# Performance work log

Measured on AMD Instinct MI355X. Metric: run time of the kernel, lower is better.

The kernel has to match this reference:

```python
import jax, jax.numpy as jnp
import numpy as np

B, T_IN, H, V, MAXLEN = 128, 256, 512, 32, 128


def gru_cell(x, h, Wih, Whh, bih, bhh):
    # torch GRU cell: gates ordered (r, z, n)
    gi = x @ Wih.T + bih            # [B, 3H]
    gh = h @ Whh.T + bhh            # [B, 3H]
    ir, iz, inn = jnp.split(gi, 3, axis=-1)
    hr, hz, hn = jnp.split(gh, 3, axis=-1)
    r = jax.nn.sigmoid(ir + hr)
    z = jax.nn.sigmoid(iz + hz)
    n = jnp.tanh(inn + r * hn)
    return (1.0 - z) * n + z * h


def run_gru_layer(xs, Wih, Whh, bih, bhh):
    # xs: [B, T, D] -> outputs [B, T, H], final hidden [B, H]
    h0 = jnp.zeros((xs.shape[0], Whh.shape[1]), xs.dtype)

    def step(h, x):
        hn = gru_cell(x, h, Wih, Whh, bih, bhh)
        return hn, hn

    hT, ys = jax.lax.scan(step, h0, jnp.swapaxes(xs, 0, 1))
    return jnp.swapaxes(ys, 0, 1), hT


def setup_inputs() -> dict:
    key = jax.random.key(0)
    ks = jax.random.split(key, 24)
    s = 1.0 / np.sqrt(H)

    def p(k, shape):
        return (jax.random.normal(k, shape, jnp.float32) * s).astype(jnp.float32)

    return {
        "x": jax.random.normal(ks[0], (B, T_IN, 2), jnp.float32),
        "emb": p(ks[1], (V, H)),
        # encoder GRU: layer0 input dim 2, layer1 input dim H
        "enc_Wih0": p(ks[2], (3 * H, 2)), "enc_Whh0": p(ks[3], (3 * H, H)),
        "enc_bih0": p(ks[4], (3 * H,)), "enc_bhh0": p(ks[5], (3 * H,)),
        "enc_Wih1": p(ks[6], (3 * H, H)), "enc_Whh1": p(ks[7], (3 * H, H)),
        "enc_bih1": p(ks[8], (3 * H,)), "enc_bhh1": p(ks[9], (3 * H,)),
        # decoder GRU: layer0 input dim 2H (embedded+context), layer1 input dim H
        "dec_Wih0": p(ks[10], (3 * H, 2 * H)), "dec_Whh0": p(ks[11], (3 * H, H)),
        "dec_bih0": p(ks[12], (3 * H,)), "dec_bhh0": p(ks[13], (3 * H,)),
        "dec_Wih1": p(ks[14], (3 * H, H)), "dec_Whh1": p(ks[15], (3 * H, H)),
        "dec_bih1": p(ks[16], (3 * H,)), "dec_bhh1": p(ks[17], (3 * H,)),
        "q_W": p(ks[18], (H, H)), "q_b": p(ks[19], (H,)),
        "out_W": p(ks[20], (V, H)), "out_b": p(ks[21], (V,)),
    }


def reference(x, emb,
              enc_Wih0, enc_Whh0, enc_bih0, enc_bhh0,
              enc_Wih1, enc_Whh1, enc_bih1, enc_bhh1,
              dec_Wih0, dec_Whh0, dec_bih0, dec_bhh0,
              dec_Wih1, dec_Whh1, dec_bih1, dec_bhh1,
              q_W, q_b, out_W, out_b):
    # ----- encoder: 2-layer GRU over trajectory points -----
    y0, h0 = run_gru_layer(x, enc_Wih0, enc_Whh0, enc_bih0, enc_bhh0)
    enc_outs, h1 = run_gru_layer(y0, enc_Wih1, enc_Whh1, enc_bih1, enc_bhh1)
    hidden0 = jnp.stack([h0, h1])                      # [L, B, H]
    bsz = x.shape[0]

    def step(carry, _):
        hidden, tok = carry                            # [L,B,H], [B] int
        embedded = emb[tok]                            # [B, H]
        query = hidden[-1] @ q_W.T + q_b               # [B, H]
        scores = jnp.einsum('bh,bth->bt', query, enc_outs)
        attn_w = jax.nn.softmax(scores, axis=-1)       # [B, T_in]
        context = jnp.einsum('bt,bth->bh', attn_w, enc_outs)
        rnn_in = jnp.concatenate([embedded, context], axis=-1)  # [B, 2H]
        g0 = gru_cell(rnn_in, hidden[0], dec_Wih0, dec_Whh0, dec_bih0, dec_bhh0)
        g1 = gru_cell(g0, hidden[1], dec_Wih1, dec_Whh1, dec_bih1, dec_bhh1)
        logits = g1 @ out_W.T + out_b                  # [B, V]
        tok_next = jnp.argmax(logits, axis=-1)
        return (jnp.stack([g0, g1]), tok_next), (logits, attn_w)

    tok0 = jnp.zeros((bsz,), jnp.int32)
    (hidden_f, _), (logits_seq, attn_seq) = jax.lax.scan(
        step, (hidden0, tok0), None, length=MAXLEN)
    vec_out = jnp.swapaxes(logits_seq, 0, 1)           # [B, max_len, V]
    attn = jnp.swapaxes(attn_seq, 0, 1)                # [B, max_len, T_in]
    return vec_out, hidden_f, attn
```

## Files before the change

kernel.cpp:

```cpp
#include <hip/hip_runtime.h>
#include <math.h>

#define BB 128
#define TT 256
#define HH 512
#define VV 32
#define MLEN 128
#define SLOT 65536

#define WT_OFF 0
#define QT_OFF 24576
#define PR_OFF 26624
#define SC_OFF 28416
#define SM_FLOATS 32512

typedef long long ll;

struct P {
    const float *x, *emb;
    const float *eWih0, *eWhh0, *ebih0, *ebhh0;
    const float *eWih1, *eWhh1, *ebih1, *ebhh1;
    const float *dWih0, *dWhh0, *dbih0, *dbhh0;
    const float *dWih1, *dWhh1, *dbih1, *dbhh1;
    const float *qW, *qb, *outW, *outb;
    float *ws;
    float *vecO, *hidO, *attnO;
};

__device__ __forceinline__ float sigf(float v) { return 1.0f / (1.0f + __expf(-v)); }

__device__ __forceinline__ float ldA(const float* p) {
    return __hip_atomic_load(p, __ATOMIC_RELAXED, __HIP_MEMORY_SCOPE_AGENT);
}
__device__ __forceinline__ void stA(float* p, float v) {
    __hip_atomic_store(p, v, __ATOMIC_RELAXED, __HIP_MEMORY_SCOPE_AGENT);
}
__device__ __forceinline__ int ldAi(const int* p) {
    return __hip_atomic_load(p, __ATOMIC_RELAXED, __HIP_MEMORY_SCOPE_AGENT);
}
__device__ __forceinline__ void stAi(int* p, int v) {
    __hip_atomic_store(p, v, __ATOMIC_RELAXED, __HIP_MEMORY_SCOPE_AGENT);
}

__device__ __forceinline__ void gbar(int* W, int target) {
    __syncthreads();
    if (threadIdx.x == 0) {
        int par = target & 1;
        int g = blockIdx.x & 15;
        int* gc = W + 32 + (par * 16 + g) * 32;
        if (__hip_atomic_fetch_add(gc, 1, __ATOMIC_RELAXED, __HIP_MEMORY_SCOPE_AGENT) == 15) {
            __hip_atomic_store(gc, 0, __ATOMIC_RELAXED, __HIP_MEMORY_SCOPE_AGENT);
            int* rc = W + 1056 + par * 32;
            if (__hip_atomic_fetch_add(rc, 1, __ATOMIC_RELAXED, __HIP_MEMORY_SCOPE_AGENT) == 15) {
                __hip_atomic_store(rc, 0, __ATOMIC_RELAXED, __HIP_MEMORY_SCOPE_AGENT);
                __hip_atomic_store(W, target, __ATOMIC_RELAXED, __HIP_MEMORY_SCOPE_AGENT);
            }
        }
        while (__hip_atomic_load(W, __ATOMIC_RELAXED, __HIP_MEMORY_SCOPE_AGENT) < target)
            __builtin_amdgcn_s_sleep(2);
    }
    __syncthreads();
}

__global__ __launch_bounds__(512, 1) void kmain(P p) {
    __shared__ __align__(16) float smu[SM_FLOATS];
    const int tid = threadIdx.x;
    const int lane = tid & 63;
    const int wv = tid >> 6;
    const int blk = blockIdx.x;

    int* W = (int*)p.ws;
    int* tok = W + 4096;
    float* f = (float*)p.ws + 8192;
    float* eh0 = f;
    float* eh1 = f + 2 * SLOT;
    float* inp = f + 4 * SLOT;
    float* qbm = f + 5 * SLOT;
    float* scoresB = f + 6 * SLOT;
    float* T = f + 6 * SLOT + SLOT / 2;
    float* xT = T + 3 * HH * VV;
    float* encO = f + (SLOT / 4) * 33;

    const float4* t4 = (const float4*)smu;
    const float4* t4q = (const float4*)(smu + QT_OFF);

    const int jg = blk >> 1;
    const int bh = blk & 1;
    const int b2 = bh * 64 + lane;
    int bar = 0;

    {
        stA(eh0 + blk * 1024 + tid, 0.0f);
        stA(eh0 + blk * 1024 + 512 + tid, 0.0f);
        if (tid < 256) {
            int idx = blk * 256 + tid;
            int t = idx >> 8, c = (idx >> 7) & 1, b = idx & 127;
            stA(xT + idx, p.x[((ll)b * TT + t) * 2 + c]);
        }
        if (tid < 192) {
            int unit = blk * 192 + tid;
            int v = unit & 31, gj = unit >> 5;
            const float* wrow = p.dWih0 + (ll)gj * 1024;
            const float* erow = p.emb + (ll)v * HH;
            float acc = 0.0f;
#pragma unroll 8
            for (int d = 0; d < HH; ++d) acc = fmaf(wrow[d], erow[d], acc);
            stA(T + unit, acc);
        }
#pragma unroll
        for (int jl = 0; jl < 4; ++jl)
            smu[QT_OFF + jl * 512 + tid] = p.qW[((ll)(jg * 4 + jl)) * HH + tid];
#pragma unroll
        for (int r = 0; r < 24; ++r) {
            int g = r >> 2, jl = r & 3, j = jg * 4 + jl;
            const float* src = (g < 3) ? (p.eWhh0 + (ll)(g * HH + j) * HH)
                                       : (p.eWih1 + (ll)((g - 3) * HH + j) * HH);
            smu[WT_OFF + r * 512 + tid] = src[tid];
        }
#pragma unroll
        for (int r = 0; r < 12; ++r) {
            int g = r >> 2, jl = r & 3, j = jg * 4 + jl;
            smu[WT_OFF + (24 + r) * 512 + tid] = p.eWhh1[(ll)(g * HH + j) * HH + tid];
        }
        gbar(W, ++bar);
    }

    for (int t = 0; t <= TT; ++t) {
        const float* h0s = eh0 + (((t + 1) & 1) ? SLOT : 0);
        float*       h0d = eh0 + ((t & 1) ? SLOT : 0);
        const float* h1s = eh1 + (((t + 1) & 1) ? SLOT : 0);
        float*       h1d = eh1 + ((t & 1) ? SLOT : 0);

        smu[PR_OFF + tid] = 0.0f;
        smu[PR_OFF + 512 + tid] = 0.0f;
        smu[PR_OFF + 1024 + tid] = 0.0f;
        if (tid < 256) smu[PR_OFF + 1536 + tid] = 0.0f;
        __syncthreads();

        {
            const int rotE = jg & 7;
            const int ds0 = wv * 64;
            float acc[36];
#pragma unroll
            for (int r = 0; r < 36; ++r) acc[r] = 0.0f;
            float av[2][8], bv[2][8];
            {
                const int d0c = ds0 + rotE * 8;
#pragma unroll
                for (int u = 0; u < 8; ++u) av[0][u] = ldA(h0s + (ll)(d0c + u) * BB + b2);
#pragma unroll
                for (int u = 0; u < 8; ++u) bv[0][u] = ldA(h1s + (ll)(d0c + u) * BB + b2);
            }
#pragma unroll
            for (int c = 0; c < 8; ++c) {
                const int cb = c & 1, pb = cb ^ 1;
                if (c < 7) {
                    const int dn = ds0 + ((c + 1 + rotE) & 7) * 8;
#pragma unroll
                    for (int u = 0; u < 8; ++u) av[pb][u] = ldA(h0s + (ll)(dn + u) * BB + b2);
#pragma unroll
                    for (int u = 0; u < 8; ++u) bv[pb][u] = ldA(h1s + (ll)(dn + u) * BB + b2);
                }
                const int db = ds0 + ((c + rotE) & 7) * 8;
#pragma unroll
                for (int h2 = 0; h2 < 2; ++h2) {
                    const int q4 = (db + h2 * 4) >> 2;
#pragma unroll
                    for (int r = 0; r < 24; ++r) {
                        float4 w = t4[r * 128 + q4];
                        acc[r] = fmaf(w.x, av[cb][h2 * 4 + 0], acc[r]);
                        acc[r] = fmaf(w.y, av[cb][h2 * 4 + 1], acc[r]);
                        acc[r] = fmaf(w.z, av[cb][h2 * 4 + 2], acc[r]);
                        acc[r] = fmaf(w.w, av[cb][h2 * 4 + 3], acc[r]);
                    }
#pragma unroll
                    for (int r = 0; r < 12; ++r) {
                        float4 w = t4[(24 + r) * 128 + q4];
                        acc[24 + r] = fmaf(w.x, bv[cb][h2 * 4 + 0], acc[24 + r]);
                        acc[24 + r] = fmaf(w.y, bv[cb][h2 * 4 + 1], acc[24 + r]);
                        acc[24 + r] = fmaf(w.z, bv[cb][h2 * 4 + 2], acc[24 + r]);
                        acc[24 + r] = fmaf(w.w, bv[cb][h2 * 4 + 3], acc[24 + r]);
                    }
                }
            }
#pragma unroll
            for (int r = 0; r < 24; ++r)
                unsafeAtomicAdd(&smu[PR_OFF + r * 64 + lane], acc[r]);
#pragma unroll
            for (int r = 0; r < 12; ++r) {
                int g = r >> 2;
                int prow = (g < 2) ? (12 + g * 4) : 24;
                unsafeAtomicAdd(&smu[PR_OFF + (prow + (r & 3)) * 64 + lane], acc[24 + r]);
            }
        }
        __syncthreads();

        if (wv < 4) {
            if (t < TT) {
                int jl = wv, j = jg * 4 + jl;
                float* pr = smu + PR_OFF;
                float hr = pr[(0 + jl) * 64 + lane] + p.ebhh0[j];
                float hz = pr[(4 + jl) * 64 + lane] + p.ebhh0[HH + j];
                float hn = pr[(8 + jl) * 64 + lane] + p.ebhh0[2 * HH + j];
                float x0 = xT[t * 256 + b2], x1 = xT[t * 256 + 128 + b2];
                float ir = fmaf(p.eWih0[j * 2], x0, fmaf(p.eWih0[j * 2 + 1], x1, p.ebih0[j]));
                float iz = fmaf(p.eWih0[(HH + j) * 2], x0, fmaf(p.eWih0[(HH + j) * 2 + 1], x1, p.ebih0[HH + j]));
                float in_ = fmaf(p.eWih0[(2 * HH + j) * 2], x0, fmaf(p.eWih0[(2 * HH + j) * 2 + 1], x1, p.ebih0[2 * HH + j]));
                float r = sigf(ir + hr), z = sigf(iz + hz);
                float n = tanhf(in_ + r * hn);
                float hp = ldA(h0s + (ll)j * BB + b2);
                stA(h0d + (ll)j * BB + b2, (1.0f - z) * n + z * hp);
            }
        } else if (t >= 1) {
            int jl = wv - 4, j = jg * 4 + jl;
            float* pr = smu + PR_OFF;
            float rs = pr[(12 + jl) * 64 + lane] + p.ebih1[j] + p.ebhh1[j];
            float zs = pr[(16 + jl) * 64 + lane] + p.ebih1[HH + j] + p.ebhh1[HH + j];
            float in1 = pr[(20 + jl) * 64 + lane] + p.ebih1[2 * HH + j];
            float hn1 = pr[(24 + jl) * 64 + lane] + p.ebhh1[2 * HH + j];
            float r = sigf(rs), z = sigf(zs);
            float n = tanhf(in1 + r * hn1);
            float hp = ldA(h1s + (ll)j * BB + b2);
            float hv = (1.0f - z) * n + z * hp;
            stA(h1d + (ll)j * BB + b2, hv);
            stA(encO + ((ll)(t - 1) * HH + j) * BB + b2, hv);
        }
        gbar(W, ++bar);
    }

    {
        const float* h1c = eh1;
        if (tid < 256) smu[PR_OFF + tid] = 0.0f;
#pragma unroll
        for (int r = 0; r < 12; ++r) {
            int g = r >> 2, jl = r & 3, j = jg * 4 + jl;
            smu[WT_OFF + r * 1024 + tid]              = p.dWih0[(ll)(g * HH + j) * 1024 + 512 + tid];
            smu[WT_OFF + r * 1024 + 512 + tid]        = p.dWhh0[(ll)(g * HH + j) * HH + tid];
            smu[WT_OFF + (12 + r) * 1024 + tid]       = p.dWih1[(ll)(g * HH + j) * HH + tid];
            smu[WT_OFF + (12 + r) * 1024 + 512 + tid] = p.dWhh1[(ll)(g * HH + j) * HH + tid];
        }
        __syncthreads();
        {
            const int ds0 = wv * 64;
            float acc[4] = {0, 0, 0, 0};
            float av[8];
            for (int c = 0; c < 8; ++c) {
                int db = ds0 + c * 8;
#pragma unroll
                for (int u = 0; u < 8; ++u) av[u] = ldA(h1c + (ll)(db + u) * BB + b2);
#pragma unroll
                for (int h2 = 0; h2 < 2; ++h2) {
                    int q4 = (db + h2 * 4) >> 2;
#pragma unroll
                    for (int jl = 0; jl < 4; ++jl) {
                        float4 w = t4q[jl * 128 + q4];
                        acc[jl] = fmaf(w.x, av[h2 * 4 + 0], acc[jl]);
                        acc[jl] = fmaf(w.y, av[h2 * 4 + 1], acc[jl]);
                        acc[jl] = fmaf(w.z, av[h2 * 4 + 2], acc[jl]);
                        acc[jl] = fmaf(w.w, av[h2 * 4 + 3], acc[jl]);
                    }
                }
            }
#pragma unroll
            for (int jl = 0; jl < 4; ++jl)
                unsafeAtomicAdd(&smu[PR_OFF + jl * 64 + lane], acc[jl]);
        }
        __syncthreads();
        if (wv < 4) {
            int j = jg * 4 + wv;
            stA(qbm + (ll)j * BB + b2, smu[PR_OFF + wv * 64 + lane] + p.qb[j]);
        }
        if (blk == 128 && tid < BB) stAi(tok + tid, 0);
        gbar(W, ++bar);
    }

    for (int s = 0; s < MLEN; ++s) {
        const float* h0s = eh0 + (((s + 1) & 1) ? SLOT : 0);
        float*       g0d = eh0 + ((s & 1) ? SLOT : 0);
        const float* h1s = eh1 + ((s & 1) ? SLOT : 0);
        float*       h1d = eh1 + (((s + 1) & 1) ? SLOT : 0);

        {
            const int rotA = jg & 7;
            const int t0 = (blk >> 1) * 2;
            if (tid < 128) smu[PR_OFF + tid] = 0.0f;
            __syncthreads();
            const int js = wv * 64;
            float a0 = 0.0f, a1 = 0.0f;
            float qv[2][8], e0[2][8], e1[2][8];
            {
                const int j0 = js + rotA * 8;
#pragma unroll
                for (int u = 0; u < 8; ++u) {
                    qv[0][u] = ldA(qbm + (ll)(j0 + u) * BB + b2);
                    e0[0][u] = encO[((ll)t0 * HH + j0 + u) * BB + b2];
                    e1[0][u] = encO[((ll)(t0 + 1) * HH + j0 + u) * BB + b2];
                }
            }
#pragma unroll
            for (int c = 0; c < 8; ++c) {
                const int cb = c & 1, pb = cb ^ 1;
                if (c < 7) {
                    const int jn = js + ((c + 1 + rotA) & 7) * 8;
#pragma unroll
                    for (int u = 0; u < 8; ++u) {
                        qv[pb][u] = ldA(qbm + (ll)(jn + u) * BB + b2);
                        e0[pb][u] = encO[((ll)t0 * HH + jn + u) * BB + b2];
                        e1[pb][u] = encO[((ll)(t0 + 1) * HH + jn + u) * BB + b2];
                    }
                }
#pragma unroll
                for (int u = 0; u < 8; ++u) {
                    a0 = fmaf(qv[cb][u], e0[cb][u], a0);
                    a1 = fmaf(qv[cb][u], e1[cb][u], a1);
                }
            }
            unsafeAtomicAdd(&smu[PR_OFF + lane], a0);
            unsafeAtomicAdd(&smu[PR_OFF + 64 + lane], a1);
            __syncthreads();
            if (wv < 2)
                stA(scoresB + (ll)(t0 + wv) * BB + b2, smu[PR_OFF + wv * 64 + lane]);
        }
        gbar(W, ++bar);

        {
            const int d0 = jg * 4;
            float sv[32];
            for (int i = 0; i < 32; ++i) {
                int k = (i + (jg & 31)) & 31;
                sv[k] = ldA(scoresB + (ll)(wv * 32 + k) * BB + b2);
            }
            if (tid < 256) smu[PR_OFF + tid] = 0.0f;
            float mp = sv[0];
#pragma unroll
            for (int k = 1; k < 32; ++k) mp = fmaxf(mp, sv[k]);
            smu[SC_OFF + wv * 64 + lane] = mp;
            __syncthreads();
            float m = smu[SC_OFF + lane];
#pragma unroll
            for (int u = 1; u < 8; ++u) m = fmaxf(m, smu[SC_OFF + u * 64 + lane]);
            float e[32], lp = 0.0f;
#pragma unroll
            for (int k = 0; k < 32; ++k) { e[k] = __expf(sv[k] - m); lp += e[k]; }
            smu[SC_OFF + 512 + wv * 64 + lane] = lp;
            __syncthreads();
            float l = smu[SC_OFF + 512 + lane];
#pragma unroll
            for (int u = 1; u < 8; ++u) l += smu[SC_OFF + 512 + u * 64 + lane];
            float rl = 1.0f / l;
            if (blk < 16 && wv == jg) {
#pragma unroll
                for (int k = 0; k < 32; ++k) smu[SC_OFF + 1024 + k * 65 + lane] = e[k] * rl;
            }
            float c4[4] = {0, 0, 0, 0};
            float ev[2][32];
#pragma unroll
            for (int u = 0; u < 8; ++u) {
                const float* Ep = encO + ((ll)(wv * 32 + u) * HH + d0) * BB + b2;
#pragma unroll
                for (int q = 0; q < 4; ++q) ev[0][u * 4 + q] = Ep[q * BB];
            }
#pragma unroll
            for (int kb = 0; kb < 4; ++kb) {
                const int cb = kb & 1, pb = cb ^ 1;
                if (kb < 3) {
#pragma unroll
                    for (int u = 0; u < 8; ++u) {
                        const float* Ep = encO + ((ll)(wv * 32 + (kb + 1) * 8 + u) * HH + d0) * BB + b2;
#pragma unroll
                        for (int q = 0; q < 4; ++q) ev[pb][u * 4 + q] = Ep[q * BB];
                    }
                }
#pragma unroll
                for (int u = 0; u < 8; ++u) {
                    const int k = kb * 8 + u;
                    c4[0] = fmaf(e[k], ev[cb][u * 4 + 0], c4[0]);
                    c4[1] = fmaf(e[k], ev[cb][u * 4 + 1], c4[1]);
                    c4[2] = fmaf(e[k], ev[cb][u * 4 + 2], c4[2]);
                    c4[3] = fmaf(e[k], ev[cb][u * 4 + 3], c4[3]);
                }
            }
#pragma unroll
            for (int kk = 0; kk < 4; ++kk)
                unsafeAtomicAdd(&smu[PR_OFF + kk * 64 + lane], c4[kk]);
            __syncthreads();
            if (tid < 256) {
                int kk = tid >> 6, ln = tid & 63;
                float l2 = smu[SC_OFF + 512 + ln];
#pragma unroll
                for (int u = 1; u < 8; ++u) l2 += smu[SC_OFF + 512 + u * 64 + ln];
                float val = smu[PR_OFF + kk * 64 + ln] / l2;
                stA(inp + (ll)(d0 + kk) * BB + bh * 64 + ln, val);
            }
            if (blk < 16) {
                int bi = tid >> 3, tj = tid & 7;
#pragma unroll
                for (int u = 0; u < 4; ++u) {
                    int tl = tj * 4 + u;
                    p.attnO[((ll)(bh * 64 + bi) * MLEN + s) * TT + jg * 32 + tl] = smu[SC_OFF + 1024 + tl * 65 + bi];
                }
            }
        }
        gbar(W, ++bar);

        {
            const int rotG = jg & 15;
            smu[PR_OFF + tid] = 0.0f;
            smu[PR_OFF + 512 + tid] = 0.0f;
            __syncthreads();
            const int ctxw = (wv < 4);
            const float* stream = ctxw ? inp : h0s;
            const int ds0 = (wv & 3) * 128;
            const int tb = ctxw ? 0 : 512;
            float acc[12];
#pragma unroll
            for (int r = 0; r < 12; ++r) acc[r] = 0.0f;
            float av[2][8];
            {
                const int d0c = ds0 + rotG * 8;
#pragma unroll
                for (int u = 0; u < 8; ++u) av[0][u] = ldA(stream + (ll)(d0c + u) * BB + b2);
            }
#pragma unroll
            for (int c = 0; c < 16; ++c) {
                const int cb = c & 1, pb = cb ^ 1;
                if (c < 15) {
                    const int dn = ds0 + ((c + 1 + rotG) & 15) * 8;
#pragma unroll
                    for (int u = 0; u < 8; ++u) av[pb][u] = ldA(stream + (ll)(dn + u) * BB + b2);
                }
                const int db = ds0 + ((c + rotG) & 15) * 8;
#pragma unroll
                for (int h2 = 0; h2 < 2; ++h2) {
                    const int q4 = (tb + db + h2 * 4) >> 2;
#pragma unroll
                    for (int r = 0; r < 12; ++r) {
                        float4 w = t4[r * 256 + q4];
                        acc[r] = fmaf(w.x, av[cb][h2 * 4 + 0], acc[r]);
                        acc[r] = fmaf(w.y, av[cb][h2 * 4 + 1], acc[r]);
                        acc[r] = fmaf(w.z, av[cb][h2 * 4 + 2], acc[r]);
                        acc[r] = fmaf(w.w, av[cb][h2 * 4 + 3], acc[r]);
                    }
                }
            }
#pragma unroll
            for (int r = 0; r < 12; ++r) {
                int g = r >> 2;
                int prow = (g < 2) ? g * 4 : (ctxw ? 8 : 12);
                unsafeAtomicAdd(&smu[PR_OFF + (prow + (r & 3)) * 64 + lane], acc[r]);
            }
            __syncthreads();
            if (wv < 4) {
                int jl = wv, j = jg * 4 + jl;
                float* pr = smu + PR_OFF;
                int tokb = ldAi(tok + b2);
                float rs = T[(ll)j * 32 + tokb] + pr[(0 + jl) * 64 + lane] + p.dbih0[j] + p.dbhh0[j];
                float zs = T[(ll)(HH + j) * 32 + tokb] + pr[(4 + jl) * 64 + lane] + p.dbih0[HH + j] + p.dbhh0[HH + j];
                float ins = T[(ll)(2 * HH + j) * 32 + tokb] + pr[(8 + jl) * 64 + lane] + p.dbih0[2 * HH + j];
                float hns = pr[(12 + jl) * 64 + lane] + p.dbhh0[2 * HH + j];
                float r = sigf(rs), z = sigf(zs);
                float n = tanhf(ins + r * hns);
                float hp = ldA(h0s + (ll)j * BB + b2);
                stA(g0d + (ll)j * BB + b2, (1.0f - z) * n + z * hp);
            }
        }
        gbar(W, ++bar);

        {
            const int rotG = jg & 15;
            smu[PR_OFF + tid] = 0.0f;
            smu[PR_OFF + 512 + tid] = 0.0f;
            __syncthreads();
            const int iw = (wv < 4);
            const float* stream = iw ? g0d : h1s;
            const int ds0 = (wv & 3) * 128;
            const int tb = iw ? 0 : 512;
            float acc[12];
#pragma unroll
            for (int r = 0; r < 12; ++r) acc[r] = 0.0f;
            float av[2][8];
            {
                const int d0c = ds0 + rotG * 8;
#pragma unroll
                for (int u = 0; u < 8; ++u) av[0][u] = ldA(stream + (ll)(d0c + u) * BB + b2);
            }
#pragma unroll
            for (int c = 0; c < 16; ++c) {
                const int cb = c & 1, pb = cb ^ 1;
                if (c < 15) {
                    const int dn = ds0 + ((c + 1 + rotG) & 15) * 8;
#pragma unroll
                    for (int u = 0; u < 8; ++u) av[pb][u] = ldA(stream + (ll)(dn + u) * BB + b2);
                }
                const int db = ds0 + ((c + rotG) & 15) * 8;
#pragma unroll
                for (int h2 = 0; h2 < 2; ++h2) {
                    const int q4 = (tb + db + h2 * 4) >> 2;
#pragma unroll
                    for (int r = 0; r < 12; ++r) {
                        float4 w = t4[(12 + r) * 256 + q4];
                        acc[r] = fmaf(w.x, av[cb][h2 * 4 + 0], acc[r]);
                        acc[r] = fmaf(w.y, av[cb][h2 * 4 + 1], acc[r]);
                        acc[r] = fmaf(w.z, av[cb][h2 * 4 + 2], acc[r]);
                        acc[r] = fmaf(w.w, av[cb][h2 * 4 + 3], acc[r]);
                    }
                }
            }
#pragma unroll
            for (int r = 0; r < 12; ++r) {
                int g = r >> 2;
                int prow = (g < 2) ? g * 4 : (iw ? 8 : 12);
                unsafeAtomicAdd(&smu[PR_OFF + (prow + (r & 3)) * 64 + lane], acc[r]);
            }
            __syncthreads();
            if (wv < 4) {
                int jl = wv, j = jg * 4 + jl;
                float* pr = smu + PR_OFF;
                float rs = pr[(0 + jl) * 64 + lane] + p.dbih1[j] + p.dbhh1[j];
                float zs = pr[(4 + jl) * 64 + lane] + p.dbih1[HH + j] + p.dbhh1[HH + j];
                float ins = pr[(8 + jl) * 64 + lane] + p.dbih1[2 * HH + j];
                float hns = pr[(12 + jl) * 64 + lane] + p.dbhh1[2 * HH + j];
                float r = sigf(rs), z = sigf(zs);
                float n = tanhf(ins + r * hns);
                float hp = ldA(h1s + (ll)j * BB + b2);
                stA(h1d + (ll)j * BB + b2, (1.0f - z) * n + z * hp);
            }
        }
        gbar(W, ++bar);

        {
            const int rotD = jg & 7;
            const float* h1c = h1d;
            if (tid < 256) smu[PR_OFF + tid] = 0.0f;
            __syncthreads();
            {
                const int ds0 = wv * 64;
                float acc4[4] = {0, 0, 0, 0};
                float av[2][8];
                {
                    const int d0c = ds0 + rotD * 8;
#pragma unroll
                    for (int u = 0; u < 8; ++u) av[0][u] = ldA(h1c + (ll)(d0c + u) * BB + b2);
                }
#pragma unroll
                for (int c = 0; c < 8; ++c) {
                    const int cb = c & 1, pb = cb ^ 1;
                    if (c < 7) {
                        const int dn = ds0 + ((c + 1 + rotD) & 7) * 8;
#pragma unroll
                        for (int u = 0; u < 8; ++u) av[pb][u] = ldA(h1c + (ll)(dn + u) * BB + b2);
                    }
                    const int db = ds0 + ((c + rotD) & 7) * 8;
#pragma unroll
                    for (int h2 = 0; h2 < 2; ++h2) {
                        const int q4 = (db + h2 * 4) >> 2;
#pragma unroll
                        for (int jl = 0; jl < 4; ++jl) {
                            float4 w = t4q[jl * 128 + q4];
                            acc4[jl] = fmaf(w.x, av[cb][h2 * 4 + 0], acc4[jl]);
                            acc4[jl] = fmaf(w.y, av[cb][h2 * 4 + 1], acc4[jl]);
                            acc4[jl] = fmaf(w.z, av[cb][h2 * 4 + 2], acc4[jl]);
                            acc4[jl] = fmaf(w.w, av[cb][h2 * 4 + 3], acc4[jl]);
                        }
                    }
                }
#pragma unroll
                for (int jl = 0; jl < 4; ++jl)
                    unsafeAtomicAdd(&smu[PR_OFF + jl * 64 + lane], acc4[jl]);
            }
            __syncthreads();
            if (wv < 4) {
                int j = jg * 4 + wv;
                stA(qbm + (ll)j * BB + b2, smu[PR_OFF + wv * 64 + lane] + p.qb[j]);
            }
            if (blk >= 128 && blk < 160) {
                __syncthreads();
                const int bb = (blk - 128) * 4;
#pragma unroll
                for (int i = 0; i < 4; ++i) {
                    int f2 = i * 512 + tid;
                    int d = f2 >> 2, bi2 = f2 & 3;
                    smu[SC_OFF + f2] = ldA(h1c + (ll)d * BB + bb + bi2);
                }
                __syncthreads();
                if (tid < 128) {
                    const int bl = tid >> 5, v = tid & 31;
                    float acc = 0.0f;
                    for (int d4 = 0; d4 < 128; ++d4) {
                        float4 w4 = *(const float4*)(p.outW + (ll)v * HH + d4 * 4);
                        acc = fmaf(w4.x, smu[SC_OFF + (d4 * 4 + 0) * 4 + bl], acc);
                        acc = fmaf(w4.y, smu[SC_OFF + (d4 * 4 + 1) * 4 + bl], acc);
                        acc = fmaf(w4.z, smu[SC_OFF + (d4 * 4 + 2) * 4 + bl], acc);
                        acc = fmaf(w4.w, smu[SC_OFF + (d4 * 4 + 3) * 4 + bl], acc);
                    }
                    acc += p.outb[v];
                    p.vecO[((ll)(bb + bl) * MLEN + s) * VV + v] = acc;
                    smu[SC_OFF + 2048 + tid] = acc;
                }
                __syncthreads();
                if (tid < 4) {
                    int base = SC_OFF + 2048 + tid * 32;
                    float best = smu[base];
                    int bi2 = 0;
#pragma unroll
                    for (int u = 1; u < 32; ++u) {
                        float val = smu[base + u];
                        if (val > best) { best = val; bi2 = u; }
                    }
                    stAi(tok + bb + tid, bi2);
                }
            }
        }
        gbar(W, ++bar);
    }

    {
        int idx = blk * 512 + tid;
        int l = idx >> 16, rr = idx & 65535;
        int b = rr >> 9, h = rr & 511;
        const float* src = l ? eh1 : (eh0 + SLOT);
        p.hidO[idx] = ldA(src + (ll)h * BB + b);
    }
}

extern "C" void kernel_launch(void* const* d_in, const int* in_sizes, int n_in,
                              void* d_out, int out_size, void* d_ws, size_t ws_size,
                              hipStream_t stream) {
    (void)in_sizes; (void)n_in; (void)out_size; (void)ws_size;
    P prm;
    prm.x     = (const float*)d_in[0];
    prm.emb   = (const float*)d_in[1];
    prm.eWih0 = (const float*)d_in[2];
    prm.eWhh0 = (const float*)d_in[3];
    prm.ebih0 = (const float*)d_in[4];
    prm.ebhh0 = (const float*)d_in[5];
    prm.eWih1 = (const float*)d_in[6];
    prm.eWhh1 = (const float*)d_in[7];
    prm.ebih1 = (const float*)d_in[8];
    prm.ebhh1 = (const float*)d_in[9];
    prm.dWih0 = (const float*)d_in[10];
    prm.dWhh0 = (const float*)d_in[11];
    prm.dbih0 = (const float*)d_in[12];
    prm.dbhh0 = (const float*)d_in[13];
    prm.dWih1 = (const float*)d_in[14];
    prm.dWhh1 = (const float*)d_in[15];
    prm.dbih1 = (const float*)d_in[16];
    prm.dbhh1 = (const float*)d_in[17];
    prm.qW    = (const float*)d_in[18];
    prm.qb    = (const float*)d_in[19];
    prm.outW  = (const float*)d_in[20];
    prm.outb  = (const float*)d_in[21];
    prm.ws    = (float*)d_ws;
    prm.vecO  = (float*)d_out;
    prm.hidO  = prm.vecO + (ll)BB * MLEN * VV;
    prm.attnO = prm.hidO + (ll)2 * BB * HH;

    hipMemsetAsync(d_ws, 0, 16384, stream);
    void* args[] = { &prm };
    hipLaunchCooperativeKernel((void*)kmain, dim3(256), dim3(512), args, 0, stream);
}
```

Before: 29.98 ms.

## Interleave hidden-state feature pairs in workspace to enable 64-bit atomic loads

Changes the workspace layout of hidden states, query, scores, context input and encoder outputs so that each pair of adjacent feature (or time) indices for a batch element sits next to each other in memory. Every strided single-float relaxed atomic load in the matvec inner loops becomes a 64-bit float2 load, halving the number of global load instructions on the recurrent critical path. Coalescing changes because a wavefront now reads 512 contiguous bytes per load, and correctness depends on every producer and consumer using the new index macros consistently.

```diff
diff --git a/kernel.cpp b/kernel.cpp
--- a/kernel.cpp
+++ b/kernel.cpp
@@ -13,6 +13,10 @@
 #define PR_OFF 26624
 #define SC_OFF 28416
 #define SM_FLOATS 32512
+
+#define HX(d, b) ((((d) >> 1) << 8) + ((b) << 1) + ((d) & 1))
+#define SX(t, b) ((((t) >> 1) << 8) + ((b) << 1) + ((t) & 1))
+#define EX(t, j, b) ((ll)(t) * (HH * BB) + (((j) >> 1) << 8) + ((b) << 1) + ((j) & 1))
 
 typedef long long ll;
 
@@ -31,6 +35,11 @@
 
 __device__ __forceinline__ float ldA(const float* p) {
     return __hip_atomic_load(p, __ATOMIC_RELAXED, __HIP_MEMORY_SCOPE_AGENT);
+}
+__device__ __forceinline__ float2 ldA2(const float* p) {
+    unsigned long long v = __hip_atomic_load((const unsigned long long*)p,
+                                             __ATOMIC_RELAXED, __HIP_MEMORY_SCOPE_AGENT);
+    union { unsigned long long u; float2 f; } c; c.u = v; return c.f;
 }
 __device__ __forceinline__ void stA(float* p, float v) {
     __hip_atomic_store(p, v, __ATOMIC_RELAXED, __HIP_MEMORY_SCOPE_AGENT);
@@ -147,9 +156,12 @@
             {
                 const int d0c = ds0 + rotE * 8;
 #pragma unroll
-                for (int u = 0; u < 8; ++u) av[0][u] = ldA(h0s + (ll)(d0c + u) * BB + b2);
-#pragma unroll
-                for (int u = 0; u < 8; ++u) bv[0][u] = ldA(h1s + (ll)(d0c + u) * BB + b2);
+                for (int k = 0; k < 4; ++k) {
+                    float2 va = ldA2(h0s + HX(d0c + 2 * k, b2));
+                    av[0][2 * k] = va.x; av[0][2 * k + 1] = va.y;
+                    float2 vb = ldA2(h1s + HX(d0c + 2 * k, b2));
+                    bv[0][2 * k] = vb.x; bv[0][2 * k + 1] = vb.y;
+                }
             }
 #pragma unroll
             for (int c = 0; c < 8; ++c) {
@@ -157,9 +169,12 @@
                 if (c < 7) {
                     const int dn = ds0 + ((c + 1 + rotE) & 7) * 8;
 #pragma unroll
-                    for (int u = 0; u < 8; ++u) av[pb][u] = ldA(h0s + (ll)(dn + u) * BB + b2);
-#pragma unroll
-                    for (int u = 0; u < 8; ++u) bv[pb][u] = ldA(h1s + (ll)(dn + u) * BB + b2);
+                    for (int k = 0; k < 4; ++k) {
+                        float2 va = ldA2(h0s + HX(dn + 2 * k, b2));
+                        av[pb][2 * k] = va.x; av[pb][2 * k + 1] = va.y;
+                        float2 vb = ldA2(h1s + HX(dn + 2 * k, b2));
+                        bv[pb][2 * k] = vb.x; bv[pb][2 * k + 1] = vb.y;
+                    }
                 }
                 const int db = ds0 + ((c + rotE) & 7) * 8;
 #pragma unroll
@@ -208,8 +223,8 @@
                 float in_ = fmaf(p.eWih0[(2 * HH + j) * 2], x0, fmaf(p.eWih0[(2 * HH + j) * 2 + 1], x1, p.ebih0[2 * HH + j]));
                 float r = sigf(ir + hr), z = sigf(iz + hz);
                 float n = tanhf(in_ + r * hn);
-                float hp = ldA(h0s + (ll)j * BB + b2);
-                stA(h0d + (ll)j * BB + b2, (1.0f - z) * n + z * hp);
+                float hp = ldA(h0s + HX(j, b2));
+                stA(h0d + HX(j, b2), (1.0f - z) * n + z * hp);
             }
         } else if (t >= 1) {
             int jl = wv - 4, j = jg * 4 + jl;
@@ -220,10 +235,10 @@
             float hn1 = pr[(24 + jl) * 64 + lane] + p.ebhh1[2 * HH + j];
             float r = sigf(rs), z = sigf(zs);
             float n = tanhf(in1 + r * hn1);
-            float hp = ldA(h1s + (ll)j * BB + b2);
+            float hp = ldA(h1s + HX(j, b2));
             float hv = (1.0f - z) * n + z * hp;
-            stA(h1d + (ll)j * BB + b2, hv);
-            stA(encO + ((ll)(t - 1) * HH + j) * BB + b2, hv);
+            stA(h1d + HX(j, b2), hv);
+            stA(encO + EX(t - 1, j, b2), hv);
         }
         gbar(W, ++bar);
     }
@@ -247,7 +262,10 @@
             for (int c = 0; c < 8; ++c) {
                 int db = ds0 + c * 8;
 #pragma unroll
-                for (int u = 0; u < 8; ++u) av[u] = ldA(h1c + (ll)(db + u) * BB + b2);
+                for (int k = 0; k < 4; ++k) {
+                    float2 v = ldA2(h1c + HX(db + 2 * k, b2));
+                    av[2 * k] = v.x; av[2 * k + 1] = v.y;
+                }
 #pragma unroll
                 for (int h2 = 0; h2 < 2; ++h2) {
                     int q4 = (db + h2 * 4) >> 2;
@@ -268,7 +286,7 @@
         __syncthreads();
         if (wv < 4) {
             int j = jg * 4 + wv;
-            stA(qbm + (ll)j * BB + b2, smu[PR_OFF + wv * 64 + lane] + p.qb[j]);
+            stA(qbm + HX(j, b2), smu[PR_OFF + wv * 64 + lane] + p.qb[j]);
         }
         if (blk == 128 && tid < BB) stAi(tok + tid, 0);
         gbar(W, ++bar);
@@ -290,11 +308,16 @@
             float qv[2][8], e0[2][8], e1[2][8];
             {
                 const int j0 = js + rotA * 8;
-#pragma unroll
-                for (int u = 0; u < 8; ++u) {
-                    qv[0][u] = ldA(qbm + (ll)(j0 + u) * BB + b2);
-                    e0[0][u] = encO[((ll)t0 * HH + j0 + u) * BB + b2];
-                    e1[0][u] = encO[((ll)(t0 + 1) * HH + j0 + u) * BB + b2];
+                const float* eb0 = encO + (ll)t0 * (HH * BB) + ((j0 >> 1) << 8) + (b2 << 1);
+                const float* eb1 = encO + (ll)(t0 + 1) * (HH * BB) + ((j0 >> 1) << 8) + (b2 << 1);
+#pragma unroll
+                for (int k = 0; k < 4; ++k) {
+                    float2 q2 = ldA2(qbm + HX(j0 + 2 * k, b2));
+                    qv[0][2 * k] = q2.x; qv[0][2 * k + 1] = q2.y;
+                    float2 v0 = *(const float2*)(eb0 + k * 256);
+                    e0[0][2 * k] = v0.x; e0[0][2 * k + 1] = v0.y;
+                    float2 v1 = *(const float2*)(eb1 + k * 256);
+                    e1[0][2 * k] = v1.x; e1[0][2 * k + 1] = v1.y;
                 }
             }
 #pragma unroll
@@ -302,11 +325,16 @@
                 const int cb = c & 1, pb = cb ^ 1;
                 if (c < 7) {
                     const int jn = js + ((c + 1 + rotA) & 7) * 8;
-#pragma unroll
-                    for (int u = 0; u < 8; ++u) {
-                        qv[pb][u] = ldA(qbm + (ll)(jn + u) * BB + b2);
-                        e0[pb][u] = encO[((ll)t0 * HH + jn + u) * BB + b2];
-                        e1[pb][u] = encO[((ll)(t0 + 1) * HH + jn + u) * BB + b2];
+                    const float* eb0 = encO + (ll)t0 * (HH * BB) + ((jn >> 1) << 8) + (b2 << 1);
+                    const float* eb1 = encO + (ll)(t0 + 1) * (HH * BB) + ((jn >> 1) << 8) + (b2 << 1);
+#pragma unroll
+                    for (int k = 0; k < 4; ++k) {
+                        float2 q2 = ldA2(qbm + HX(jn + 2 * k, b2));
+                        qv[pb][2 * k] = q2.x; qv[pb][2 * k + 1] = q2.y;
+                        float2 v0 = *(const float2*)(eb0 + k * 256);
+                        e0[pb][2 * k] = v0.x; e0[pb][2 * k + 1] = v0.y;
+                        float2 v1 = *(const float2*)(eb1 + k * 256);
+                        e1[pb][2 * k] = v1.x; e1[pb][2 * k + 1] = v1.y;
                     }
                 }
 #pragma unroll
@@ -319,16 +347,17 @@
             unsafeAtomicAdd(&smu[PR_OFF + 64 + lane], a1);
             __syncthreads();
             if (wv < 2)
-                stA(scoresB + (ll)(t0 + wv) * BB + b2, smu[PR_OFF + wv * 64 + lane]);
+                stA(scoresB + SX(t0 + wv, b2), smu[PR_OFF + wv * 64 + lane]);
         }
         gbar(W, ++bar);
 
         {
             const int d0 = jg * 4;
             float sv[32];
-            for (int i = 0; i < 32; ++i) {
-                int k = (i + (jg & 31)) & 31;
-                sv[k] = ldA(scoresB + (ll)(wv * 32 + k) * BB + b2);
+#pragma unroll
+            for (int kp = 0; kp < 16; ++kp) {
+                float2 v = ldA2(scoresB + ((wv * 16 + kp) << 8) + (b2 << 1));
+                sv[2 * kp] = v.x; sv[2 * kp + 1] = v.y;
             }
             if (tid < 256) smu[PR_OFF + tid] = 0.0f;
             float mp = sv[0];
@@ -356,9 +385,11 @@
             float ev[2][32];
 #pragma unroll
             for (int u = 0; u < 8; ++u) {
-                const float* Ep = encO + ((ll)(wv * 32 + u) * HH + d0) * BB + b2;
-#pragma unroll
-                for (int q = 0; q < 4; ++q) ev[0][u * 4 + q] = Ep[q * BB];
+                const float* Ep = encO + (ll)(wv * 32 + u) * (HH * BB) + ((d0 >> 1) << 8) + (b2 << 1);
+                float2 pa = *(const float2*)(Ep);
+                float2 pb2 = *(const float2*)(Ep + 256);
+                ev[0][u * 4 + 0] = pa.x; ev[0][u * 4 + 1] = pa.y;
+                ev[0][u * 4 + 2] = pb2.x; ev[0][u * 4 + 3] = pb2.y;
             }
 #pragma unroll
             for (int kb = 0; kb < 4; ++kb) {
@@ -366,9 +397,11 @@
                 if (kb < 3) {
 #pragma unroll
                     for (int u = 0; u < 8; ++u) {
-                        const float* Ep = encO + ((ll)(wv * 32 + (kb + 1) * 8 + u) * HH + d0) * BB + b2;
-#pragma unroll
-                        for (int q = 0; q < 4; ++q) ev[pb][u * 4 + q] = Ep[q * BB];
+                        const float* Ep = encO + (ll)(wv * 32 + (kb + 1) * 8 + u) * (HH * BB) + ((d0 >> 1) << 8) + (b2 << 1);
+                        float2 pa = *(const float2*)(Ep);
+                        float2 pb2 = *(const float2*)(Ep + 256);
+                        ev[pb][u * 4 + 0] = pa.x; ev[pb][u * 4 + 1] = pa.y;
+                        ev[pb][u * 4 + 2] = pb2.x; ev[pb][u * 4 + 3] = pb2.y;
                     }
                 }
 #pragma unroll
@@ -390,7 +423,7 @@
 #pragma unroll
                 for (int u = 1; u < 8; ++u) l2 += smu[SC_OFF + 512 + u * 64 + ln];
                 float val = smu[PR_OFF + kk * 64 + ln] / l2;
-                stA(inp + (ll)(d0 + kk) * BB + bh * 64 + ln, val);
+                stA(inp + HX(d0 + kk, bh * 64 + ln), val);
             }
             if (blk < 16) {
                 int bi = tid >> 3, tj = tid & 7;
@@ -419,7 +452,10 @@
             {
                 const int d0c = ds0 + rotG * 8;
 #pragma unroll
-                for (int u = 0; u < 8; ++u) av[0][u] = ldA(stream + (ll)(d0c + u) * BB + b2);
+                for (int k = 0; k < 4; ++k) {
+                    float2 v = ldA2(stream + HX(d0c + 2 * k, b2));
+                    av[0][2 * k] = v.x; av[0][2 * k + 1] = v.y;
+                }
             }
 #pragma unroll
             for (int c = 0; c < 16; ++c) {
@@ -427,7 +463,10 @@
                 if (c < 15) {
                     const int dn = ds0 + ((c + 1 + rotG) & 15) * 8;
 #pragma unroll
-                    for (int u = 0; u < 8; ++u) av[pb][u] = ldA(stream + (ll)(dn + u) * BB + b2);
+                    for (int k = 0; k < 4; ++k) {
+                        float2 v = ldA2(stream + HX(dn + 2 * k, b2));
+                        av[pb][2 * k] = v.x; av[pb][2 * k + 1] = v.y;
+                    }
                 }
                 const int db = ds0 + ((c + rotG) & 15) * 8;
 #pragma unroll
@@ -460,8 +499,8 @@
                 float hns = pr[(12 + jl) * 64 + lane] + p.dbhh0[2 * HH + j];
                 float r = sigf(rs), z = sigf(zs);
                 float n = tanhf(ins + r * hns);
-                float hp = ldA(h0s + (ll)j * BB + b2);
-                stA(g0d + (ll)j * BB + b2, (1.0f - z) * n + z * hp);
+                float hp = ldA(h0s + HX(j, b2));
+                stA(g0d + HX(j, b2), (1.0f - z) * n + z * hp);
             }
         }
         gbar(W, ++bar);
@@ -482,7 +521,10 @@
             {
                 const int d0c = ds0 + rotG * 8;
 #pragma unroll
-                for (int u = 0; u < 8; ++u) av[0][u] = ldA(stream + (ll)(d0c + u) * BB + b2);
+                for (int k = 0; k < 4; ++k) {
+                    float2 v = ldA2(stream + HX(d0c + 2 * k, b2));
+                    av[0][2 * k] = v.x; av[0][2 * k + 1] = v.y;
+                }
             }
 #pragma unroll
             for (int c = 0; c < 16; ++c) {
@@ -490,7 +532,10 @@
                 if (c < 15) {
                     const int dn = ds0 + ((c + 1 + rotG) & 15) * 8;
 #pragma unroll
-                    for (int u = 0; u < 8; ++u) av[pb][u] = ldA(stream + (ll)(dn + u) * BB + b2);
+                    for (int k = 0; k < 4; ++k) {
+                        float2 v = ldA2(stream + HX(dn + 2 * k, b2));
+                        av[pb][2 * k] = v.x; av[pb][2 * k + 1] = v.y;
+                    }
                 }
                 const int db = ds0 + ((c + rotG) & 15) * 8;
 #pragma unroll
@@ -522,8 +567,8 @@
                 float hns = pr[(12 + jl) * 64 + lane] + p.dbhh1[2 * HH + j];
                 float r = sigf(rs), z = sigf(zs);
                 float n = tanhf(ins + r * hns);
-                float hp = ldA(h1s + (ll)j * BB + b2);
-                stA(h1d + (ll)j * BB + b2, (1.0f - z) * n + z * hp);
+                float hp = ldA(h1s + HX(j, b2));
+                stA(h1d + HX(j, b2), (1.0f - z) * n + z * hp);
             }
         }
         gbar(W, ++bar);
@@ -540,7 +585,10 @@
                 {
                     const int d0c = ds0 + rotD * 8;
 #pragma unroll
-                    for (int u = 0; u < 8; ++u) av[0][u] = ldA(h1c + (ll)(d0c + u) * BB + b2);
+                    for (int k = 0; k < 4; ++k) {
+                        float2 v = ldA2(h1c + HX(d0c + 2 * k, b2));
+                        av[0][2 * k] = v.x; av[0][2 * k + 1] = v.y;
+                    }
                 }
 #pragma unroll
                 for (int c = 0; c < 8; ++c) {
@@ -548,7 +596,10 @@
                     if (c < 7) {
                         const int dn = ds0 + ((c + 1 + rotD) & 7) * 8;
 #pragma unroll
-                        for (int u = 0; u < 8; ++u) av[pb][u] = ldA(h1c + (ll)(dn + u) * BB + b2);
+                        for (int k = 0; k < 4; ++k) {
+                            float2 v = ldA2(h1c + HX(dn + 2 * k, b2));
+                            av[pb][2 * k] = v.x; av[pb][2 * k + 1] = v.y;
+                        }
                     }
                     const int db = ds0 + ((c + rotD) & 7) * 8;
 #pragma unroll
@@ -571,7 +622,7 @@
             __syncthreads();
             if (wv < 4) {
                 int j = jg * 4 + wv;
-                stA(qbm + (ll)j * BB + b2, smu[PR_OFF + wv * 64 + lane] + p.qb[j]);
+                stA(qbm + HX(j, b2), smu[PR_OFF + wv * 64 + lane] + p.qb[j]);
             }
             if (blk >= 128 && blk < 160) {
                 __syncthreads();
@@ -580,7 +631,7 @@
                 for (int i = 0; i < 4; ++i) {
                     int f2 = i * 512 + tid;
                     int d = f2 >> 2, bi2 = f2 & 3;
-                    smu[SC_OFF + f2] = ldA(h1c + (ll)d * BB + bb + bi2);
+                    smu[SC_OFF + f2] = ldA(h1c + HX(d, bb + bi2));
                 }
                 __syncthreads();
                 if (tid < 128) {
@@ -619,7 +670,7 @@
         int l = idx >> 16, rr = idx & 65535;
         int b = rr >> 9, h = rr & 511;
         const float* src = l ? eh1 : (eh0 + SLOT);
-        p.hidO[idx] = ldA(src + (ll)h * BB + b);
+        p.hidO[idx] = ldA(src + HX(h, b));
     }
 }
 
```

Result: no change. 29.45 ms (-1.8%).
